# Kernel tuning notes

Hardware: AMD Instinct MI355X
Metric: run time of the kernel (lower is better)

Reference implementation:

```python
import jax, jax.numpy as jnp
import numpy as np

B, T, S, A = 4, 10, 6, 6
HID, L, IMG = 512, 6, 128
NCH = 16  # spatial-softmax channels
_px, _py = np.meshgrid(np.linspace(-1.0, 1.0, IMG), np.linspace(-1.0, 1.0, IMG))
POSX = jnp.asarray(_px.reshape(-1), jnp.float32)
POSY = jnp.asarray(_py.reshape(-1), jnp.float32)


def _conv_relu(x, w, b):
    y = jax.lax.conv_general_dilated(x, w, (1, 1), 'SAME',
                                     dimension_numbers=('NCHW', 'OIHW', 'NCHW'))
    return jax.nn.relu(y + b[None, :, None, None])


def _cnn_ss(x, ws, bs):
    for w, b in zip(ws, bs):
        x = _conv_relu(x, w, b)
    n = x.shape[0]
    attn = jax.nn.softmax(x.reshape(n, NCH, -1), axis=-1)  # (n, 16, H*W)
    ex = attn @ POSX  # (n, 16)
    ey = attn @ POSY
    return jnp.stack([ex, ey], axis=-1).reshape(n, 2 * NCH)  # (n, 32)


def _lstm_cell(x, h, c, wih, whh, bih, bhh):
    g = x @ wih.T + bih + h @ whh.T + bhh
    i, f, gg, o = jnp.split(g, 4, axis=-1)  # torch LSTMCell gate order i,f,g,o
    c2 = jax.nn.sigmoid(f) * c + jax.nn.sigmoid(i) * jnp.tanh(gg)
    h2 = jax.nn.sigmoid(o) * jnp.tanh(c2)
    return h2, c2


def setup_inputs() -> dict:
    key = jax.random.key(0)
    ks = iter(jax.random.split(key, 64))

    def nrm(shape, s=0.05):
        return jax.random.normal(next(ks), shape, dtype=jnp.float32) * s

    inp = {
        'seq_img_main': nrm((B, T, 3, IMG, IMG), 1.0),
        'seq_img_secondary': nrm((B, T, 3, IMG, IMG), 1.0),
        'seq_states': nrm((B, T, S), 1.0),
    }
    chans = [(32, 3), (64, 32), (128, 64), (16, 128)]
    for cam in ('m', 's'):
        for j, (o, ci) in enumerate(chans):
            inp[f'{cam}_w{j}'] = nrm((o, ci, 3, 3))
            inp[f'{cam}_b{j}'] = nrm((o,))
    in0, inr = S + 64, HID + 64  # 70 and 576
    inp['wih0'] = nrm((4 * HID, in0)); inp['whh0'] = nrm((4 * HID, HID))
    inp['bih0'] = nrm((4 * HID,)); inp['bhh0'] = nrm((4 * HID,))
    inp['wih_r'] = nrm((L - 1, 4 * HID, inr)); inp['whh_r'] = nrm((L - 1, 4 * HID, HID))
    inp['bih_r'] = nrm((L - 1, 4 * HID)); inp['bhh_r'] = nrm((L - 1, 4 * HID))
    inp['out_w'] = nrm((A, inr)); inp['out_b'] = nrm((A,))
    return inp


def reference(seq_img_main, seq_img_secondary, seq_states,
              m_w0, m_b0, m_w1, m_b1, m_w2, m_b2, m_w3, m_b3,
              s_w0, s_b0, s_w1, s_b1, s_w2, s_b2, s_w3, s_b3,
              wih0, whh0, bih0, bhh0, wih_r, whh_r, bih_r, bhh_r,
              out_w, out_b):
    b, t = seq_img_main.shape[:2]
    fm = _cnn_ss(seq_img_main.reshape(b * t, 3, IMG, IMG),
                 [m_w0, m_w1, m_w2, m_w3], [m_b0, m_b1, m_b2, m_b3])
    fs = _cnn_ss(seq_img_secondary.reshape(b * t, 3, IMG, IMG),
                 [s_w0, s_w1, s_w2, s_w3], [s_b0, s_b1, s_b2, s_b3])
    img = jnp.concatenate([fm, fs], axis=-1).reshape(b, t, 64)  # (B,T,64)

    h0 = jnp.zeros((L, b, HID), jnp.float32)
    c0 = jnp.zeros((L, b, HID), jnp.float32)

    def step(carry, xt):
        h, c = carry
        st, im = xt  # (B,S), (B,64)
        x = jnp.concatenate([st, im], axis=-1)
        hn, cn = _lstm_cell(x, h[0], c[0], wih0, whh0, bih0, bhh0)
        hs, cs = [hn], [cn]
        for l in range(L - 1):
            x = jnp.concatenate([hs[-1], im], axis=-1)
            hl, cl = _lstm_cell(x, h[l + 1], c[l + 1],
                                wih_r[l], whh_r[l], bih_r[l], bhh_r[l])
            hs.append(hl); cs.append(cl)
        out = jnp.concatenate([hs[-1], im], axis=-1) @ out_w.T + out_b
        return (jnp.stack(hs), jnp.stack(cs)), out

    _, outs = jax.lax.scan(step, (h0, c0),
                           (seq_states.transpose(1, 0, 2), img.transpose(1, 0, 2)))
    return outs.transpose(1, 0, 2)  # (B,T,A)
```

## Files before the change

### kernel.cpp

```cpp
#include <hip/hip_runtime.h>
#include <hip/hip_bf16.h>
#include <math.h>

typedef __hip_bfloat16 bf16;
typedef short bf16x8 __attribute__((ext_vector_type(8)));
typedef float f32x4 __attribute__((ext_vector_type(4)));

static constexpr int HWPX = 16384;
static constexpr int NBL  = 64;

__device__ inline float sigmoidf_(float x) { return 1.0f / (1.0f + expf(-x)); }
__device__ inline float bflo(unsigned u) { return __uint_as_float(u << 16); }
__device__ inline float bfhi(unsigned u) { return __uint_as_float(u & 0xffff0000u); }
__device__ inline int swz(int x) { return (x ^ (x >> 2)) & 3; }

__device__ inline void gll16(const bf16* g, short* l) {
    __builtin_amdgcn_global_load_lds(
        (const __attribute__((address_space(1))) void*)g,
        (__attribute__((address_space(3))) void*)l, 16, 0, 0);
}

__device__ inline int flag_peek(int* p) {
    return __hip_atomic_load(p, __ATOMIC_RELAXED, __HIP_MEMORY_SCOPE_AGENT);
}
__device__ inline void flag_post(int* p) {
    __syncthreads();
    if (threadIdx.x == 0)
        __hip_atomic_fetch_add(p, 1, __ATOMIC_RELAXED, __HIP_MEMORY_SCOPE_AGENT);
}
__device__ inline float devload(const float* p) {
    return __hip_atomic_load(p, __ATOMIC_RELAXED, __HIP_MEMORY_SCOPE_AGENT);
}
__device__ inline void devstore(float* p, float v) {
    __hip_atomic_store(p, v, __ATOMIC_RELAXED, __HIP_MEMORY_SCOPE_AGENT);
}

__global__ __launch_bounds__(256) void prep_lstm_k(
    const float* __restrict__ wih0, const float* __restrict__ whh0,
    const float* __restrict__ wihr, const float* __restrict__ whhr,
    bf16* __restrict__ d0, bf16* __restrict__ d1,
    bf16* __restrict__ d2, bf16* __restrict__ d3)
{
    const size_t nA = 2048ull * 72, nB = 2048ull * 512;
    const size_t nC = 5ull * 2048 * 576, nD = 5ull * 2048 * 512;
    for (size_t i = blockIdx.x * 256ull + threadIdx.x; i < nA + nB + nC + nD;
         i += (size_t)gridDim.x * 256) {
        if (i < nA) {
            int c = (int)(i % 72), r = (int)(i / 72);
            d0[i] = __float2bfloat16(c < 70 ? wih0[(size_t)r * 70 + c] : 0.f);
        } else if (i < nA + nB) {
            size_t k = i - nA; d1[k] = __float2bfloat16(whh0[k]);
        } else if (i < nA + nB + nC) {
            size_t k = i - nA - nB; d2[k] = __float2bfloat16(wihr[k]);
        } else {
            size_t k = i - nA - nB - nC; d3[k] = __float2bfloat16(whhr[k]);
        }
    }
}

struct ConvW {
    const float* src[8];
    bf16* dst[8];
};

__global__ __launch_bounds__(256) void prep_conv_k(ConvW a)
{
    const int sizes[4] = {3072, 18432, 73728, 18432};
    const int cins[4] = {3, 32, 64, 128};
    const int couts[4] = {32, 64, 128, 16};
    int total = 2 * 113664;
    for (int idx = blockIdx.x * 256 + threadIdx.x; idx < total; idx += gridDim.x * 256) {
        int i = idx, cam = 0;
        if (i >= 113664) { cam = 1; i -= 113664; }
        int layer = 0;
        while (layer < 3 && i >= sizes[layer]) { i -= sizes[layer]; ++layer; }
        const float* w = a.src[cam * 4 + layer];
        bf16* d = a.dst[cam * 4 + layer];
        if (layer == 0) {
            int k = i & 31, co = (i >> 5) & 31, ky = i >> 10;
            int kx = k >> 3, c = k & 7;
            float v = (kx < 3 && c < 3) ? w[((co * 3 + c) * 3 + ky) * 3 + kx] : 0.f;
            d[i] = __float2bfloat16(v);
        } else {
            int CIN = cins[layer], COUT = couts[layer], KC = CIN / 32;
            int e = i & 7;
            int t2 = i >> 3;
            int co = t2 % COUT;
            int t3 = t2 / COUT;
            int q = t3 & 3;
            int t4 = t3 >> 2;
            int kc = t4 % KC;
            int tap = t4 / KC;
            d[i] = __float2bfloat16(w[((size_t)(co * CIN + kc * 32 + q * 8 + e)) * 9 + tap]);
        }
    }
}

__global__ __launch_bounds__(256) void conv0_nhwc(
    const float* __restrict__ srcm, const float* __restrict__ srcs,
    const bf16* __restrict__ w0m, const bf16* __restrict__ w0s,
    const float* __restrict__ bm, const float* __restrict__ bs,
    bf16* __restrict__ out, int c0)
{
    const int y = blockIdx.x;
    const int cam = blockIdx.y;
    const int img = blockIdx.z;
    const int ci_ = cam * gridDim.z + img;
    const float* inImg = (cam ? srcs : srcm) + (size_t)(c0 + img) * 3 * HWPX;
    const bf16* wT0 = cam ? w0s : w0m;
    const float* bias = cam ? bs : bm;
    const int tid = threadIdx.x;
    const int wave = tid >> 6, lane = tid & 63;
    const int wm = wave & 1, wn = wave >> 1;
    const int q = lane >> 4, n16 = lane & 15;

    __shared__ short smem[3 * 130 * 16];

    for (int d = tid; d < 3 * 130; d += 256) {
        int x = d % 130, r = d / 130;
        int yy = y + r - 1, xx = x - 1;
        bf16 v8[8];
#pragma unroll
        for (int c = 0; c < 8; ++c) v8[c] = __float2bfloat16(0.f);
        if ((unsigned)yy < 128u && (unsigned)xx < 128u) {
            int o = yy * 128 + xx;
            v8[0] = __float2bfloat16(inImg[o]);
            v8[1] = __float2bfloat16(inImg[HWPX + o]);
            v8[2] = __float2bfloat16(inImg[2 * HWPX + o]);
        }
        *(bf16x8*)(void*)&smem[(r * 130 + x) * 16] = *(bf16x8*)(void*)v8;
        *(bf16x8*)(void*)&smem[(r * 130 + x) * 16 + 8] = (bf16x8)0;
    }
    __syncthreads();

    f32x4 acc[4];
#pragma unroll
    for (int nt = 0; nt < 4; ++nt) acc[nt] = f32x4{0.f, 0.f, 0.f, 0.f};

    const int co = wm * 16 + n16;
#pragma unroll
    for (int ky = 0; ky < 3; ++ky) {
        bf16x8 aF = *(const bf16x8*)(const void*)(wT0 + ((size_t)(ky * 32 + co) * 32) + q * 8);
#pragma unroll
        for (int nt = 0; nt < 4; ++nt) {
            int x = (wn * 4 + nt) * 16 + n16;
            int off = (q < 3) ? (ky * 130 + x + q) * 16 : (ky * 130 + x) * 16 + 8;
            bf16x8 bF = *(const bf16x8*)(const void*)&smem[off];
            acc[nt] = __builtin_amdgcn_mfma_f32_16x16x32_bf16(aF, bF, acc[nt], 0, 0, 0);
        }
    }

    int co0 = wm * 16 + q * 4;
#pragma unroll
    for (int nt = 0; nt < 4; ++nt) {
        int x = (wn * 4 + nt) * 16 + n16;
        bf16 tmp[4];
#pragma unroll
        for (int r = 0; r < 4; ++r) {
            float v = acc[nt][r] + bias[co0 + r];
            tmp[r] = __float2bfloat16(v > 0.f ? v : 0.f);
        }
        *reinterpret_cast<uint2*>(out + ((size_t)ci_ * HWPX + y * 128 + x) * 32 + co0)
            = *reinterpret_cast<uint2*>(tmp);
    }
}

template <int CIN, int COUT>
__global__ __launch_bounds__(256, 4) void conv2r(
    const bf16* __restrict__ in, const bf16* __restrict__ wTm,
    const bf16* __restrict__ wTs, const float* __restrict__ bm,
    const float* __restrict__ bs, bf16* __restrict__ out,
    const char* __restrict__ zpage)
{
    constexpr int KC = CIN / 32;
    constexpr int NB = (KC > 1) ? 2 : 1;
    constexpr int MW = COUT / 32;
    constexpr int SLOTS = 4 * 264;

    const int y0 = (blockIdx.x >> 1) * 2;
    const int x0 = (blockIdx.x & 1) * 64;
    const int cam = blockIdx.y;
    const int img = blockIdx.z;
    const int ci_ = cam * gridDim.z + img;
    const bf16* wT = cam ? wTs : wTm;
    const float* bias = cam ? bs : bm;
    const int tid = threadIdx.x;
    const int wave = tid >> 6, lane = tid & 63;
    const int wrow = wave >> 1, wm = wave & 1;
    const int q = lane >> 4, n16 = lane & 15;

    __shared__ short smem[NB][SLOTS * 8];
    const bf16* inImg = in + (size_t)ci_ * HWPX * CIN;

    const bf16* sptr[5];
#pragma unroll
    for (int it = 0; it < 5; ++it) {
        int s = it * 256 + tid;
        int r = s / 264, s2 = s - r * 264;
        int sx = s2 >> 2;
        int g = (s2 & 3) ^ swz(sx);
        int yy = y0 + r - 1, xx = x0 + sx - 1;
        bool ok = (s < SLOTS) && ((unsigned)yy < 128u) && ((unsigned)xx < 128u);
        sptr[it] = ok ? inImg + ((size_t)yy * 128 + xx) * CIN + g * 8
                      : (const bf16*)(zpage + (tid & 255) * 16);
    }
    auto stage = [&](int kc, int buf) {
#pragma unroll
        for (int it = 0; it < 5; ++it) {
            if (it * 256 + tid < SLOTS)
                gll16(sptr[it] + kc * 32, &smem[buf][it * 2048 + wave * 512]);
        }
    };

    f32x4 acc[MW][4];
#pragma unroll
    for (int mt = 0; mt < MW; ++mt)
#pragma unroll
        for (int nt = 0; nt < 4; ++nt) acc[mt][nt] = f32x4{0.f, 0.f, 0.f, 0.f};

    stage(0, 0);
    for (int kc = 0; kc < KC; ++kc) {
        __syncthreads();
        if (kc + 1 < KC) stage(kc + 1, (kc + 1) % NB);
        const short* sb = smem[kc % NB];
#pragma unroll
        for (int ky = 0; ky < 3; ++ky) {
#pragma unroll
            for (int kx = 0; kx < 3; ++kx) {
                bf16x8 aF[MW];
#pragma unroll
                for (int mt = 0; mt < MW; ++mt) {
                    int co = (wm * MW + mt) * 16 + n16;
                    aF[mt] = *(const bf16x8*)(const void*)(wT +
                        ((((size_t)(ky * 3 + kx) * KC + kc) * 4 + q) * COUT + co) * 8);
                }
#pragma unroll
                for (int nt = 0; nt < 4; ++nt) {
                    int xt = nt * 16 + n16 + kx;
                    int slot = (wrow + ky) * 264 + xt * 4 + (q ^ swz(xt));
                    bf16x8 bF = *(const bf16x8*)(const void*)&sb[slot * 8];
#pragma unroll
                    for (int mt = 0; mt < MW; ++mt)
                        acc[mt][nt] = __builtin_amdgcn_mfma_f32_16x16x32_bf16(
                            aF[mt], bF, acc[mt][nt], 0, 0, 0);
                }
            }
        }
    }

    const int y = y0 + wrow;
#pragma unroll
    for (int mt = 0; mt < MW; ++mt) {
        int co0 = (wm * MW + mt) * 16 + q * 4;
#pragma unroll
        for (int nt = 0; nt < 4; ++nt) {
            int x = x0 + nt * 16 + n16;
            bf16 tmp[4];
#pragma unroll
            for (int r = 0; r < 4; ++r) {
                float v = acc[mt][nt][r] + bias[co0 + r];
                tmp[r] = __float2bfloat16(v > 0.f ? v : 0.f);
            }
            *reinterpret_cast<uint2*>(out + ((size_t)ci_ * HWPX + y * 128 + x) * COUT + co0)
                = *reinterpret_cast<uint2*>(tmp);
        }
    }
}

__global__ __launch_bounds__(256, 6) void conv4_xs(
    const bf16* __restrict__ in, const bf16* __restrict__ wTm,
    const bf16* __restrict__ wTs, const float* __restrict__ bm,
    const float* __restrict__ bs,
    float* __restrict__ partial,
    const char* __restrict__ zpage, int c0)
{
    constexpr int CIN = 128, COUT = 16, KC = 4;
    constexpr int SLOTS = 3 * 66 * 4;
    const int y = blockIdx.x >> 1;
    const int xh = blockIdx.x & 1;
    const int x0 = xh * 64;
    const int cam = blockIdx.y;
    const int img = blockIdx.z;
    const int ci_ = cam * gridDim.z + img;
    const int gimg = cam * 40 + c0 + img;
    const bf16* wT = cam ? wTs : wTm;
    const float* bias = cam ? bs : bm;
    const int tid = threadIdx.x;
    const int wave = tid >> 6, lane = tid & 63;
    const int q = lane >> 4, n16 = lane & 15;

    __shared__ short smem[2][SLOTS * 8];
    __shared__ float sred[3][4][16];
    const bf16* inImg = in + (size_t)ci_ * HWPX * CIN;

    const bf16* sptr[4];
#pragma unroll
    for (int it = 0; it < 4; ++it) {
        int s = it * 256 + tid;
        int r = s / 264, s2 = s - r * 264;
        int sx = s2 >> 2;
        int g = (s2 & 3) ^ swz(sx);
        int yy = y + r - 1, xx = x0 + sx - 1;
        bool ok = (s < SLOTS) && ((unsigned)yy < 128u) && ((unsigned)xx < 128u);
        sptr[it] = ok ? inImg + ((size_t)yy * 128 + xx) * CIN + g * 8
                      : (const bf16*)(zpage + (tid & 255) * 16);
    }
    auto stage = [&](int kc, int buf) {
#pragma unroll
        for (int it = 0; it < 4; ++it) {
            if (it * 256 + tid < SLOTS)
                gll16(sptr[it] + kc * 32, &smem[buf][it * 2048 + wave * 512]);
        }
    };

    f32x4 acc = f32x4{0.f, 0.f, 0.f, 0.f};

    stage(0, 0);
    for (int kc = 0; kc < KC; ++kc) {
        __syncthreads();
        if (kc + 1 < KC) stage(kc + 1, (kc + 1) & 1);
        const short* sb = smem[kc & 1];
#pragma unroll
        for (int ky = 0; ky < 3; ++ky) {
#pragma unroll
            for (int kx = 0; kx < 3; ++kx) {
                bf16x8 aF = *(const bf16x8*)(const void*)(wT +
                    ((((size_t)(ky * 3 + kx) * KC + kc) * 4 + q) * COUT + n16) * 8);
                int xt = wave * 16 + n16 + kx;
                int slot = xt * 4 + (q ^ swz(xt));
                bf16x8 bF = *(const bf16x8*)(const void*)&sb[ky * 2112 + slot * 8];
                acc = __builtin_amdgcn_mfma_f32_16x16x32_bf16(aF, bF, acc, 0, 0, 0);
            }
        }
    }

    float v[4];
    int x = x0 + wave * 16 + n16;
    float px = -1.f + (2.f / 127.f) * x;
#pragma unroll
    for (int r = 0; r < 4; ++r) {
        float t = acc[r] + bias[q * 4 + r];
        v[r] = t > 0.f ? t : 0.f;
    }
    float M[4];
#pragma unroll
    for (int r = 0; r < 4; ++r) {
        M[r] = v[r];
        M[r] = fmaxf(M[r], __shfl_xor(M[r], 1));
        M[r] = fmaxf(M[r], __shfl_xor(M[r], 2));
        M[r] = fmaxf(M[r], __shfl_xor(M[r], 4));
        M[r] = fmaxf(M[r], __shfl_xor(M[r], 8));
    }
    if (n16 == 0)
#pragma unroll
        for (int r = 0; r < 4; ++r) sred[0][wave][q * 4 + r] = M[r];
    __syncthreads();
#pragma unroll
    for (int r = 0; r < 4; ++r) {
        M[r] = fmaxf(fmaxf(sred[0][0][q * 4 + r], sred[0][1][q * 4 + r]),
                     fmaxf(sred[0][2][q * 4 + r], sred[0][3][q * 4 + r]));
    }
    float s[4], sx[4];
#pragma unroll
    for (int r = 0; r < 4; ++r) {
        float e = expf(v[r] - M[r]);
        s[r] = e; sx[r] = e * px;
        s[r] += __shfl_xor(s[r], 1);  sx[r] += __shfl_xor(sx[r], 1);
        s[r] += __shfl_xor(s[r], 2);  sx[r] += __shfl_xor(sx[r], 2);
        s[r] += __shfl_xor(s[r], 4);  sx[r] += __shfl_xor(sx[r], 4);
        s[r] += __shfl_xor(s[r], 8);  sx[r] += __shfl_xor(sx[r], 8);
    }
    __syncthreads();
    if (n16 == 0)
#pragma unroll
        for (int r = 0; r < 4; ++r) {
            sred[1][wave][q * 4 + r] = s[r];
            sred[2][wave][q * 4 + r] = sx[r];
        }
    __syncthreads();
    if (tid < 16) {
        float S = sred[1][0][tid] + sred[1][1][tid] + sred[1][2][tid] + sred[1][3][tid];
        float SX = sred[2][0][tid] + sred[2][1][tid] + sred[2][2][tid] + sred[2][3][tid];
        float Mv = fmaxf(fmaxf(sred[0][0][tid], sred[0][1][tid]),
                         fmaxf(sred[0][2][tid], sred[0][3][tid]));
        float* pp = partial + (((size_t)gimg * 16 + tid) * 256 + (y * 2 + xh)) * 4;
        pp[0] = Mv; pp[1] = S; pp[2] = SX;
    }
}

__global__ __launch_bounds__(256) void ssmerge_k(
    const float* __restrict__ partial, float* __restrict__ featm,
    float* __restrict__ feats)
{
    const int img = blockIdx.x;
    const int cam = img / 40, li = img % 40;
    float* feat = cam ? feats : featm;
    const int tid = threadIdx.x;
    const int co = tid >> 4, s = tid & 15;
    const float* base = partial + ((size_t)img * 16 + co) * 256 * 4;
    float M = -1e30f, S = 0.f, SX = 0.f, SY = 0.f;
    for (int i = s; i < 256; i += 16) {
        float m = base[i * 4], sv = base[i * 4 + 1], sxv = base[i * 4 + 2];
        float py = -1.f + (2.f / 127.f) * (i >> 1);
        float Mn = fmaxf(M, m);
        float w0 = expf(M - Mn), w1 = expf(m - Mn);
        S = S * w0 + sv * w1;
        SX = SX * w0 + sxv * w1;
        SY = SY * w0 + sv * py * w1;
        M = Mn;
    }
#pragma unroll
    for (int mask = 1; mask < 16; mask <<= 1) {
        float Mo = __shfl_xor(M, mask), So = __shfl_xor(S, mask);
        float SXo = __shfl_xor(SX, mask), SYo = __shfl_xor(SY, mask);
        float Mn = fmaxf(M, Mo);
        float w0 = expf(M - Mn), w1 = expf(Mo - Mn);
        S = S * w0 + So * w1; SX = SX * w0 + SXo * w1; SY = SY * w0 + SYo * w1;
        M = Mn;
    }
    if (s == 0) {
        feat[(size_t)li * 32 + 2 * co] = SX / S;
        feat[(size_t)li * 32 + 2 * co + 1] = SY / S;
    }
}

__device__ inline float imgfeat(const float* featm, const float* feats,
                                int b, int t, int k)
{
    int idx = (b * 10 + t) * 32;
    return k < 32 ? featm[idx + k] : feats[idx + k - 32];
}

__global__ __launch_bounds__(256) void lstm_pipe_k(
    const bf16* __restrict__ wih0p, const bf16* __restrict__ whh0b,
    const bf16* __restrict__ wihrb, const bf16* __restrict__ whhrb,
    const float* __restrict__ bih0, const float* __restrict__ bhh0,
    const float* __restrict__ bihr, const float* __restrict__ bhhr,
    const float* __restrict__ states,
    const float* __restrict__ featm, const float* __restrict__ feats,
    float* __restrict__ hAll, float* __restrict__ cAll,
    const float* __restrict__ out_w, const float* __restrict__ out_b,
    float* __restrict__ out, int* __restrict__ cnt)
{
    const int gb = blockIdx.x;
    const int tid = threadIdx.x;

    if (gb == 6 * NBL) {
        for (int t = 0; t < 10; ++t) {
            if (tid == 0) {
                while (flag_peek(&cnt[(5 * 10 + t) * 32]) < NBL)
                    __builtin_amdgcn_s_sleep(1);
            }
            __syncthreads();
            float* h5 = hAll + ((size_t)(t + 1) * 6 + 5) * 2048;
            int p = tid >> 3, sub = tid & 7;
            if (p < 24) {
                int b = p / 6, a = p % 6;
                const float* wr = out_w + a * 576;
                float acc = 0.f;
                for (int k = sub; k < 512; k += 8) acc += wr[k] * devload(&h5[b * 512 + k]);
                for (int k = sub; k < 64; k += 8)
                    acc += wr[512 + k] * imgfeat(featm, feats, b, t, k);
                acc += __shfl_xor(acc, 1);
                acc += __shfl_xor(acc, 2);
                acc += __shfl_xor(acc, 4);
                if (sub == 0) out[(b * 10 + t) * 6 + a] = acc + out_b[a];
            }
        }
        return;
    }

    const int l = gb / NBL;
    const int bx = gb % NBL;

    const bf16 *wih, *whh;
    const float *bih, *bhh;
    int K1;
    if (l == 0) { wih = wih0p; whh = whh0b; bih = bih0; bhh = bhh0; K1 = 72; }
    else {
        wih = wihrb + (size_t)(l - 1) * 2048 * 576;
        whh = whhrb + (size_t)(l - 1) * 2048 * 512;
        bih = bihr + (l - 1) * 2048;
        bhh = bhhr + (l - 1) * 2048;
        K1 = 576;
    }
    const int XS = K1 + 512;
    float* cst = cAll + (size_t)l * 2048;

    const int b = tid >> 6;
    const int lane = tid & 63;
    const int jloc = lane >> 3;
    const int sub = lane & 7;
    const int j = bx * 8 + jloc;
    const int nb1 = K1 >> 3;

    __shared__ float xs[4 * 1088];

    for (int t = 0; t < 10; ++t) {
        if (tid == 0) {
            if (t > 0)
                while (flag_peek(&cnt[(l * 10 + t - 1) * 32]) < NBL)
                    __builtin_amdgcn_s_sleep(1);
            if (l > 0)
                while (flag_peek(&cnt[((l - 1) * 10 + t) * 32]) < NBL)
                    __builtin_amdgcn_s_sleep(1);
        }
        __syncthreads();

        float* hprev = (l == 0) ? nullptr
                     : hAll + ((size_t)(t + 1) * 6 + (l - 1)) * 2048;
        float* hold  = hAll + ((size_t)t * 6 + l) * 2048;
        float* hnew  = hAll + ((size_t)(t + 1) * 6 + l) * 2048;

        for (int i = tid; i < 4 * XS; i += 256) {
            int bb = i / XS, k = i - bb * XS;
            float v;
            if (k < K1) {
                if (hprev) v = (k < 512) ? devload(&hprev[bb * 512 + k])
                                         : imgfeat(featm, feats, bb, t, k - 512);
                else       v = (k < 6) ? states[(bb * 10 + t) * 6 + k]
                                       : (k < 70 ? imgfeat(featm, feats, bb, t, k - 6) : 0.f);
            } else {
                v = devload(&hold[bb * 512 + (k - K1)]);
            }
            xs[bb * XS + k] = v;
        }
        __syncthreads();

        const float* xb = xs + b * XS;
        const float* hp = xb + K1;
        float dg[4] = {0.f, 0.f, 0.f, 0.f};
#pragma unroll
        for (int r = 0; r < 4; ++r) {
            const uint4* w1 = reinterpret_cast<const uint4*>(wih + (size_t)(j + r * 512) * K1);
            for (int g = sub; g < nb1; g += 8) {
                uint4 u = w1[g]; const float* xp = xb + g * 8;
                dg[r] += bflo(u.x) * xp[0] + bfhi(u.x) * xp[1] + bflo(u.y) * xp[2] + bfhi(u.y) * xp[3]
                       + bflo(u.z) * xp[4] + bfhi(u.z) * xp[5] + bflo(u.w) * xp[6] + bfhi(u.w) * xp[7];
            }
            const uint4* w2 = reinterpret_cast<const uint4*>(whh + (size_t)(j + r * 512) * 512);
            for (int g = sub; g < 64; g += 8) {
                uint4 u = w2[g]; const float* xp = hp + g * 8;
                dg[r] += bflo(u.x) * xp[0] + bfhi(u.x) * xp[1] + bflo(u.y) * xp[2] + bfhi(u.y) * xp[3]
                       + bflo(u.z) * xp[4] + bfhi(u.z) * xp[5] + bflo(u.w) * xp[6] + bfhi(u.w) * xp[7];
            }
        }
#pragma unroll
        for (int r = 0; r < 4; ++r) {
            dg[r] += __shfl_xor(dg[r], 1);
            dg[r] += __shfl_xor(dg[r], 2);
            dg[r] += __shfl_xor(dg[r], 4);
        }
        if (sub == 0) {
            float gi = dg[0] + bih[j] + bhh[j];
            float gf = dg[1] + bih[j + 512] + bhh[j + 512];
            float gg = dg[2] + bih[j + 1024] + bhh[j + 1024];
            float go = dg[3] + bih[j + 1536] + bhh[j + 1536];
            float cp = cst[b * 512 + j];
            float c2 = sigmoidf_(gf) * cp + sigmoidf_(gi) * tanhf(gg);
            float h2 = sigmoidf_(go) * tanhf(c2);
            cst[b * 512 + j] = c2;
            devstore(&hnew[b * 512 + j], h2);
        }
        flag_post(&cnt[(l * 10 + t) * 32]);
    }
}

extern "C" void kernel_launch(void* const* d_in, const int* in_sizes, int n_in,
                              void* d_out, int out_size, void* d_ws, size_t ws_size,
                              hipStream_t stream)
{
    const float* seq_m = (const float*)d_in[0];
    const float* seq_s = (const float*)d_in[1];
    const float* states = (const float*)d_in[2];
    const float *cw[2][4], *cb[2][4];
    for (int cam = 0; cam < 2; ++cam)
        for (int j = 0; j < 4; ++j) {
            cw[cam][j] = (const float*)d_in[3 + cam * 8 + j * 2];
            cb[cam][j] = (const float*)d_in[3 + cam * 8 + j * 2 + 1];
        }
    const float* wih0  = (const float*)d_in[19];
    const float* whh0  = (const float*)d_in[20];
    const float* bih0  = (const float*)d_in[21];
    const float* bhh0  = (const float*)d_in[22];
    const float* wih_r = (const float*)d_in[23];
    const float* whh_r = (const float*)d_in[24];
    const float* bih_r = (const float*)d_in[25];
    const float* bhh_r = (const float*)d_in[26];
    const float* out_w = (const float*)d_in[27];
    const float* out_b = (const float*)d_in[28];
    float* out = (float*)d_out;

    char* wsc = (char*)d_ws;
    auto carve = [&](size_t bytes) {
        char* p = wsc;
        wsc += (bytes + 255) & ~(size_t)255;
        return p;
    };
    float* featm = (float*)carve(40 * 32 * 4);
    float* feats = (float*)carve(40 * 32 * 4);
    float* hAll  = (float*)carve((size_t)11 * 6 * 2048 * 4);
    float* cAll  = (float*)carve((size_t)6 * 2048 * 4);
    char*  zpage = carve(8192);
    int*   lcnt  = (int*)carve((size_t)6 * 10 * 32 * 4);
    float* partial = (float*)carve((size_t)80 * 16 * 256 * 4 * 4);
    const int wtElts[4] = {3072, 18432, 73728, 18432};
    bf16* wT[2][4];
    for (int cam = 0; cam < 2; ++cam)
        for (int j = 0; j < 4; ++j) wT[cam][j] = (bf16*)carve(wtElts[j] * 2);
    bf16* wih0p = (bf16*)carve((size_t)2048 * 72 * 2);
    bf16* whh0b = (bf16*)carve((size_t)2048 * 512 * 2);
    bf16* wihrb = (bf16*)carve((size_t)5 * 2048 * 576 * 2);
    bf16* whhrb = (bf16*)carve((size_t)5 * 2048 * 512 * 2);

    size_t used = (size_t)(wsc - (char*)d_ws);
    size_t rem = ws_size > used ? ws_size - used : 0;
    int CHI = 1;
    const int cands[7] = {20, 10, 8, 5, 4, 2, 1};
    for (int i = 0; i < 7; ++i) {
        size_t need = (size_t)2 * cands[i] * (128 + 64) * HWPX * 2;
        if (need <= rem) { CHI = cands[i]; break; }
    }
    bf16* bufA = (bf16*)carve((size_t)2 * CHI * HWPX * 128 * 2);
    bf16* bufB = (bf16*)carve((size_t)2 * CHI * HWPX * 64 * 2);

    hipMemsetAsync(hAll, 0, 6 * 2048 * 4, stream);
    hipMemsetAsync(cAll, 0, 6 * 2048 * 4, stream);
    hipMemsetAsync(zpage, 0, 8192, stream);
    hipMemsetAsync(lcnt, 0, 6 * 10 * 32 * 4, stream);

    prep_lstm_k<<<2048, 256, 0, stream>>>(wih0, whh0, wih_r, whh_r,
                                          wih0p, whh0b, wihrb, whhrb);
    ConvW cwArg;
    for (int cam = 0; cam < 2; ++cam)
        for (int j = 0; j < 4; ++j) {
            cwArg.src[cam * 4 + j] = cw[cam][j];
            cwArg.dst[cam * 4 + j] = wT[cam][j];
        }
    prep_conv_k<<<888, 256, 0, stream>>>(cwArg);

    for (int c0 = 0; c0 < 40; c0 += CHI) {
        int ch = (40 - c0) < CHI ? (40 - c0) : CHI;
        conv0_nhwc<<<dim3(128, 2, ch), 256, 0, stream>>>(
            seq_m, seq_s, wT[0][0], wT[1][0], cb[0][0], cb[1][0], bufA, c0);
        conv2r<32, 64><<<dim3(128, 2, ch), 256, 0, stream>>>(
            bufA, wT[0][1], wT[1][1], cb[0][1], cb[1][1], bufB, zpage);
        conv2r<64, 128><<<dim3(128, 2, ch), 256, 0, stream>>>(
            bufB, wT[0][2], wT[1][2], cb[0][2], cb[1][2], bufA, zpage);
        conv4_xs<<<dim3(256, 2, ch), 256, 0, stream>>>(
            bufA, wT[0][3], wT[1][3], cb[0][3], cb[1][3], partial, zpage, c0);
    }
    ssmerge_k<<<80, 256, 0, stream>>>(partial, featm, feats);

    lstm_pipe_k<<<dim3(6 * NBL + 1), 256, 0, stream>>>(
        wih0p, whh0b, wihrb, whhrb, bih0, bhh0, bih_r, bhh_r,
        states, featm, feats, hAll, cAll, out_w, out_b, out, lcnt);
}
```

Baseline: 1.279 ms.

## Replace shared atomic counters with per-block step flags in LSTM pipeline

Each LSTM block now stores its completed timestep into its own flag slot instead of atomically incrementing one shared counter per layer and step. Waiters poll all 64 producer flags in parallel, one lane per flag. The h-state loads into shared memory are also widened to 64-bit atomic loads, with a specialized fill path per layer type. The goal is to cut atomic contention and polling latency on the serial LSTM critical path, at the cost of more polling traffic.

Measured after the change: 1.234 ms. 3.5% less time.

```diff
diff --git a/kernel.cpp b/kernel.cpp
--- a/kernel.cpp
+++ b/kernel.cpp
@@ -20,16 +20,18 @@
         (__attribute__((address_space(3))) void*)l, 16, 0, 0);
 }
 
-__device__ inline int flag_peek(int* p) {
+__device__ inline int flag_ld(const int* p) {
     return __hip_atomic_load(p, __ATOMIC_RELAXED, __HIP_MEMORY_SCOPE_AGENT);
 }
-__device__ inline void flag_post(int* p) {
-    __syncthreads();
-    if (threadIdx.x == 0)
-        __hip_atomic_fetch_add(p, 1, __ATOMIC_RELAXED, __HIP_MEMORY_SCOPE_AGENT);
+__device__ inline void flag_st(int* p, int v) {
+    __hip_atomic_store(p, v, __ATOMIC_RELAXED, __HIP_MEMORY_SCOPE_AGENT);
 }
 __device__ inline float devload(const float* p) {
     return __hip_atomic_load(p, __ATOMIC_RELAXED, __HIP_MEMORY_SCOPE_AGENT);
+}
+__device__ inline unsigned long long devload2(const float* p) {
+    return __hip_atomic_load((const unsigned long long*)p,
+                             __ATOMIC_RELAXED, __HIP_MEMORY_SCOPE_AGENT);
 }
 __device__ inline void devstore(float* p, float v) {
     __hip_atomic_store(p, v, __ATOMIC_RELAXED, __HIP_MEMORY_SCOPE_AGENT);
@@ -440,25 +442,29 @@
     const float* __restrict__ featm, const float* __restrict__ feats,
     float* __restrict__ hAll, float* __restrict__ cAll,
     const float* __restrict__ out_w, const float* __restrict__ out_b,
-    float* __restrict__ out, int* __restrict__ cnt)
+    float* __restrict__ out, int* __restrict__ fl)
 {
     const int gb = blockIdx.x;
     const int tid = threadIdx.x;
 
     if (gb == 6 * NBL) {
         for (int t = 0; t < 10; ++t) {
-            if (tid == 0) {
-                while (flag_peek(&cnt[(5 * 10 + t) * 32]) < NBL)
+            if (tid < 64) {
+                while (flag_ld(&fl[5 * 64 + tid]) < t + 1)
                     __builtin_amdgcn_s_sleep(1);
             }
             __syncthreads();
-            float* h5 = hAll + ((size_t)(t + 1) * 6 + 5) * 2048;
+            const float* h5 = hAll + ((size_t)(t + 1) * 6 + 5) * 2048;
             int p = tid >> 3, sub = tid & 7;
             if (p < 24) {
                 int b = p / 6, a = p % 6;
                 const float* wr = out_w + a * 576;
                 float acc = 0.f;
-                for (int k = sub; k < 512; k += 8) acc += wr[k] * devload(&h5[b * 512 + k]);
+                for (int k = sub; k < 256; k += 8) {
+                    union { unsigned long long u; float f[2]; } cv;
+                    cv.u = devload2(&h5[b * 512 + k * 2]);
+                    acc += wr[k * 2] * cv.f[0] + wr[k * 2 + 1] * cv.f[1];
+                }
                 for (int k = sub; k < 64; k += 8)
                     acc += wr[512 + k] * imgfeat(featm, feats, b, t, k);
                 acc += __shfl_xor(acc, 1);
@@ -497,33 +503,48 @@
     __shared__ float xs[4 * 1088];
 
     for (int t = 0; t < 10; ++t) {
-        if (tid == 0) {
-            if (t > 0)
-                while (flag_peek(&cnt[(l * 10 + t - 1) * 32]) < NBL)
-                    __builtin_amdgcn_s_sleep(1);
-            if (l > 0)
-                while (flag_peek(&cnt[((l - 1) * 10 + t) * 32]) < NBL)
-                    __builtin_amdgcn_s_sleep(1);
+        if (l > 0 && tid < 64) {
+            while (flag_ld(&fl[(l - 1) * 64 + tid]) < t + 1)
+                __builtin_amdgcn_s_sleep(1);
+        }
+        if (t > 0 && tid >= 64 && tid < 128) {
+            while (flag_ld(&fl[l * 64 + (tid - 64)]) < t)
+                __builtin_amdgcn_s_sleep(1);
         }
         __syncthreads();
 
-        float* hprev = (l == 0) ? nullptr
-                     : hAll + ((size_t)(t + 1) * 6 + (l - 1)) * 2048;
-        float* hold  = hAll + ((size_t)t * 6 + l) * 2048;
-        float* hnew  = hAll + ((size_t)(t + 1) * 6 + l) * 2048;
-
-        for (int i = tid; i < 4 * XS; i += 256) {
-            int bb = i / XS, k = i - bb * XS;
-            float v;
-            if (k < K1) {
-                if (hprev) v = (k < 512) ? devload(&hprev[bb * 512 + k])
-                                         : imgfeat(featm, feats, bb, t, k - 512);
-                else       v = (k < 6) ? states[(bb * 10 + t) * 6 + k]
-                                       : (k < 70 ? imgfeat(featm, feats, bb, t, k - 6) : 0.f);
-            } else {
-                v = devload(&hold[bb * 512 + (k - K1)]);
-            }
-            xs[bb * XS + k] = v;
+        const float* hprev = (l == 0) ? nullptr
+                           : hAll + ((size_t)(t + 1) * 6 + (l - 1)) * 2048;
+        const float* hold  = hAll + ((size_t)t * 6 + l) * 2048;
+        float* hnew        = hAll + ((size_t)(t + 1) * 6 + l) * 2048;
+
+        if (l > 0) {
+            for (int i = tid; i < 4 * 512; i += 256) {
+                int bb = i >> 9, kk = i & 511;
+                union { unsigned long long u; float f[2]; } cv;
+                int base;
+                if (kk < 256) { cv.u = devload2(&hprev[bb * 512 + kk * 2]); base = bb * XS + kk * 2; }
+                else { cv.u = devload2(&hold[bb * 512 + (kk - 256) * 2]); base = bb * XS + 576 + (kk - 256) * 2; }
+                xs[base] = cv.f[0]; xs[base + 1] = cv.f[1];
+            }
+            if (tid < 256) {
+                int bb = tid >> 6, k = tid & 63;
+                xs[bb * XS + 512 + k] = imgfeat(featm, feats, bb, t, k);
+            }
+        } else {
+            for (int i = tid; i < 4 * 256; i += 256) {
+                int bb = i >> 8, kk = i & 255;
+                union { unsigned long long u; float f[2]; } cv;
+                cv.u = devload2(&hold[bb * 512 + kk * 2]);
+                int base = bb * XS + 72 + kk * 2;
+                xs[base] = cv.f[0]; xs[base + 1] = cv.f[1];
+            }
+            for (int i = tid; i < 4 * 72; i += 256) {
+                int bb = i / 72, k = i - bb * 72;
+                float v = (k < 6) ? states[(bb * 10 + t) * 6 + k]
+                                  : (k < 70 ? imgfeat(featm, feats, bb, t, k - 6) : 0.f);
+                xs[bb * XS + k] = v;
+            }
         }
         __syncthreads();
 
@@ -562,7 +583,8 @@
             cst[b * 512 + j] = c2;
             devstore(&hnew[b * 512 + j], h2);
         }
-        flag_post(&cnt[(l * 10 + t) * 32]);
+        __syncthreads();
+        if (tid == 0) flag_st(&fl[l * 64 + bx], t + 1);
     }
 }
 
@@ -602,7 +624,7 @@
     float* hAll  = (float*)carve((size_t)11 * 6 * 2048 * 4);
     float* cAll  = (float*)carve((size_t)6 * 2048 * 4);
     char*  zpage = carve(8192);
-    int*   lcnt  = (int*)carve((size_t)6 * 10 * 32 * 4);
+    int*   lcnt  = (int*)carve((size_t)6 * 64 * 4);
     float* partial = (float*)carve((size_t)80 * 16 * 256 * 4 * 4);
     const int wtElts[4] = {3072, 18432, 73728, 18432};
     bf16* wT[2][4];
@@ -627,7 +649,7 @@
     hipMemsetAsync(hAll, 0, 6 * 2048 * 4, stream);
     hipMemsetAsync(cAll, 0, 6 * 2048 * 4, stream);
     hipMemsetAsync(zpage, 0, 8192, stream);
-    hipMemsetAsync(lcnt, 0, 6 * 10 * 32 * 4, stream);
+    hipMemsetAsync(lcnt, 0, 6 * 64 * 4, stream);
 
     prep_lstm_k<<<2048, 256, 0, stream>>>(wih0, whh0, wih_r, whh_r,
                                           wih0p, whh0b, wihrb, whhrb);
```
